# Performance work log

Hardware: AMD Instinct MI355X
Metric: run time of the kernel (lower is better)

## Reference

```python
import math
import jax, jax.numpy as jnp
import numpy as np

B = 128          # graphs per batch
N = 1024         # nodes per graph
E = 1048576      # total edges (avg degree 8)
F_IN = 64
NHID = 64
NCLS = 10
RATIO = 0.8


def setup_inputs() -> dict:
    key = jax.random.key(0)
    ks = jax.random.split(key, 24)
    x = jax.random.normal(ks[0], (B * N, F_IN), jnp.float32)
    # intra-graph random edges: graph id per edge, local src/dst
    epg = E // B
    gid = jnp.repeat(jnp.arange(B, dtype=jnp.int32), epg)
    src = gid * N + jax.random.randint(ks[1], (E,), 0, N, jnp.int32)
    dst = gid * N + jax.random.randint(ks[2], (E,), 0, N, jnp.int32)
    def lin(k, fi, fo):
        s = 1.0 / np.sqrt(fi)
        return jax.random.uniform(k, (fi, fo), jnp.float32, -s, s)
    p = {
        'W1': lin(ks[3], F_IN, NHID), 'b1': jnp.zeros((NHID,), jnp.float32),
        'Wp1': lin(ks[4], NHID, 1), 'bp1': jnp.zeros((1,), jnp.float32),
        'W2': lin(ks[5], NHID, NHID), 'b2': jnp.zeros((NHID,), jnp.float32),
        'Wp2': lin(ks[6], NHID, 1), 'bp2': jnp.zeros((1,), jnp.float32),
        'W3': lin(ks[7], NHID, NHID), 'b3': jnp.zeros((NHID,), jnp.float32),
        'Wp3': lin(ks[8], NHID, 1), 'bp3': jnp.zeros((1,), jnp.float32),
        'L1w': lin(ks[9], 2 * NHID, NHID), 'L1b': jnp.zeros((NHID,), jnp.float32),
        'L2w': lin(ks[10], NHID, NHID // 2), 'L2b': jnp.zeros((NHID // 2,), jnp.float32),
        'L3w': lin(ks[11], NHID // 2, NCLS), 'L3b': jnp.zeros((NCLS,), jnp.float32),
    }
    return dict(x=x, edge_src=src, edge_dst=dst, **p)


def gcn_conv(x, W, b, src, dst, emask, n):
    # PyG GCNConv: add self loops, symmetric deg normalization
    xw = x @ W
    ew = emask.astype(x.dtype)
    deg = jax.ops.segment_sum(ew, dst, num_segments=n) + 1.0  # +1 self loop
    dis = jax.lax.rsqrt(deg)
    norm = dis[src] * dis[dst] * ew
    agg = jax.ops.segment_sum(xw[src] * norm[:, None], dst, num_segments=n)
    agg = agg + xw * (dis * dis)[:, None]  # self-loop message
    return agg + b


def sag_pool(x, Wp, bp, src, dst, emask, n_cur):
    n_tot = B * n_cur
    k = int(math.ceil(RATIO * n_cur))
    score = gcn_conv(x, Wp, bp, src, dst, emask, n_tot)[:, 0]
    _, idx = jax.lax.top_k(score.reshape(B, n_cur), k)
    perm = (idx + (jnp.arange(B, dtype=jnp.int32) * n_cur)[:, None]).reshape(-1)
    xn = x[perm] * jnp.tanh(score[perm])[:, None]
    new_idx = jnp.full((n_tot,), -1, jnp.int32).at[perm].set(
        jnp.arange(B * k, dtype=jnp.int32))
    ns, nd = new_idx[src], new_idx[dst]
    valid = emask & (ns >= 0) & (nd >= 0)
    return xn, jnp.where(valid, ns, 0), jnp.where(valid, nd, 0), valid, k


def readout(x, k):
    xr = x.reshape(B, k, NHID)
    return jnp.concatenate([xr.max(axis=1), xr.mean(axis=1)], axis=1)


def reference(x, edge_src, edge_dst, W1, b1, Wp1, bp1, W2, b2, Wp2, bp2,
              W3, b3, Wp3, bp3, L1w, L1b, L2w, L2b, L3w, L3b):
    src = edge_src.astype(jnp.int32)
    dst = edge_dst.astype(jnp.int32)
    emask = jnp.ones((E,), bool)
    n = N
    h = jax.nn.relu(gcn_conv(x, W1, b1, src, dst, emask, B * n))
    h, src, dst, emask, n = sag_pool(h, Wp1, bp1, src, dst, emask, n)
    r1 = readout(h, n)
    h = jax.nn.relu(gcn_conv(h, W2, b2, src, dst, emask, B * n))
    h, src, dst, emask, n = sag_pool(h, Wp2, bp2, src, dst, emask, n)
    r2 = readout(h, n)
    h = jax.nn.relu(gcn_conv(h, W3, b3, src, dst, emask, B * n))
    h, src, dst, emask, n = sag_pool(h, Wp3, bp3, src, dst, emask, n)
    r3 = readout(h, n)
    z = r1 + r2 + r3
    z = jax.nn.relu(z @ L1w + L1b)          # dropout is identity in eval
    z = jax.nn.relu(z @ L2w + L2b)
    return jax.nn.log_softmax(z @ L3w + L3b, axis=-1)
```

## Files before the change

kernel.cpp:

```cpp
#include <hip/hip_runtime.h>
#include <math.h>

constexpr int B_  = 128;
constexpr int N_  = 1024;
constexpr int E_  = 1048576;
constexpr int BN_ = B_ * N_;
constexpr int EPG = E_ / B_;
constexpr int NSEG = 16;

typedef short v8s __attribute__((ext_vector_type(8)));
typedef float v4f __attribute__((ext_vector_type(4)));

__device__ __forceinline__ unsigned bf16_rne(unsigned u) {
    return (u + 0x7FFFu + ((u >> 16) & 1u)) >> 16;
}

__global__ __launch_bounds__(1024) void k_csr2(
        const int* __restrict__ src, const int* __restrict__ dst,
        const int* __restrict__ cum,
        int* __restrict__ srt, int* __restrict__ rowptr,
        float* __restrict__ dis, int n) {
    __shared__ int cnt[1024];
    __shared__ int cur[1024];
    __shared__ int cums[1024];
    __shared__ int wsum[17];
    int g = blockIdx.x, tid = threadIdx.x;
    int gb   = g * N_;
    int base = g * n;
    const int eb = g * EPG;

    cums[tid] = cum ? cum[gb + tid] : tid;
    cnt[tid] = 0;
    __syncthreads();
    for (int t = tid; t < EPG; t += 1024) {
        int s = cums[src[eb + t] - gb];
        int d = cums[dst[eb + t] - gb];
        if ((s | d) >= 0) atomicAdd(&cnt[d], 1);
    }
    __syncthreads();

    int c = (tid < n) ? cnt[tid] : 0;
    int v = c;
    int lane = tid & 63, wv = tid >> 6;
    #pragma unroll
    for (int off = 1; off < 64; off <<= 1) {
        int t = __shfl_up(v, off, 64);
        if (lane >= off) v += t;
    }
    if (lane == 63) wsum[wv] = v;
    __syncthreads();
    if (tid == 0) {
        int run = 0;
        #pragma unroll
        for (int i = 0; i < 16; ++i) { int t = wsum[i]; wsum[i] = run; run += t; }
        wsum[16] = run;
    }
    __syncthreads();
    int excl = v - c + wsum[wv];
    if (tid < n) {
        cur[tid] = excl;
        rowptr[g * (n + 1) + tid] = excl;
        dis[base + tid] = rsqrtf((float)c + 1.0f);
    }
    if (tid == 0) rowptr[g * (n + 1) + n] = wsum[16];
    __syncthreads();

    for (int t = tid; t < EPG; t += 1024) {
        int s = cums[src[eb + t] - gb];
        int d = cums[dst[eb + t] - gb];
        if ((s | d) < 0) continue;
        int pos = atomicAdd(&cur[d], 1);
        srt[eb + pos] = s;
    }
}

__global__ __launch_bounds__(1024) void k_wprep3(
        const float* __restrict__ W0, const float* __restrict__ W1,
        const float* __restrict__ W2, unsigned short* __restrict__ wfall) {
    const float* W = (blockIdx.x == 0) ? W0 : (blockIdx.x == 1) ? W1 : W2;
    unsigned short* wf = wfall + (size_t)blockIdx.x * 8192;
    int t = threadIdx.x;
    int l  = t & 63;
    int kk = (t >> 6) & 1;
    int c  = (t >> 7) & 3;
    int p  = (t >> 9) & 1;
    int col = c * 16 + (l & 15);
    int kbase = kk * 32 + (l >> 4) * 8;
    unsigned short o[8];
    #pragma unroll
    for (int j = 0; j < 8; ++j) {
        float w = W[(kbase + j) * 64 + col];
        unsigned u  = __float_as_uint(w);
        unsigned hi = bf16_rne(u);
        if (p == 0) o[j] = (unsigned short)hi;
        else {
            float lo = w - __uint_as_float(hi << 16);
            o[j] = (unsigned short)bf16_rne(__float_as_uint(lo));
        }
    }
    uint4 v;
    v.x = o[0] | ((unsigned)o[1] << 16);
    v.y = o[2] | ((unsigned)o[3] << 16);
    v.z = o[4] | ((unsigned)o[5] << 16);
    v.w = o[6] | ((unsigned)o[7] << 16);
    *reinterpret_cast<uint4*>(wf + (size_t)t * 8) = v;
}

__global__ __launch_bounds__(1024) void k_conv(
        const int* __restrict__ srt, const int* __restrict__ rowptr,
        const float* __restrict__ dis, const float* __restrict__ h,
        const int* __restrict__ perm, const float* __restrict__ ggate,
        const unsigned short* __restrict__ wf,
        const float* __restrict__ bias, const float* __restrict__ Wp,
        float* __restrict__ hout, float* __restrict__ saggq,
        int n, int rows) {
    extern __shared__ float lds[];
    float* xs   = lds;
    float* ps   = xs + n * 20;
    int*   lrp  = (int*)(ps + n);
    int*   lsrt = lrp + (n + 4);
    float* hs   = (float*)(lsrt + EPG);
    float* sdis = hs + 128 * 68;

    int g = blockIdx.x & 127, q = blockIdx.x >> 7;
    int foff = q * 16;
    int tid  = threadIdx.x;
    int base = g * n;

    for (int i = tid; i <= n; i += 1024) lrp[i] = rowptr[g * (n + 1) + i];
    __syncthreads();
    int total = lrp[n];
    const int* gsrt = srt + g * EPG;
    for (int i = tid; i < total; i += 1024) lsrt[i] = gsrt[i];

    int lane = tid & 63;
    v8s wh[2], wl[2];
    #pragma unroll
    for (int kk = 0; kk < 2; ++kk) {
        wh[kk] = *reinterpret_cast<const v8s*>(wf + (((size_t)((0*4 + q)*2 + kk))*64 + lane)*8);
        wl[kk] = *reinterpret_cast<const v8s*>(wf + (((size_t)((1*4 + q)*2 + kk))*64 + lane)*8);
    }

    int wave = tid >> 6;
    int m = lane & 15, b = lane >> 4;
    for (int c0 = 0; c0 < n; c0 += 128) {
        int ric = min(128, n - c0);
        __syncthreads();
        for (int i = tid; i < 128 * 16; i += 1024) {
            int row = i >> 4, s = i & 15;
            float4 v = {0.f, 0.f, 0.f, 0.f};
            if (row < ric) {
                if (perm) {
                    int pr   = perm[base + c0 + row];
                    float gt = ggate[base + c0 + row];
                    v = *reinterpret_cast<const float4*>(h + (size_t)pr * 64 + s * 4);
                    v.x *= gt; v.y *= gt; v.z *= gt; v.w *= gt;
                } else {
                    v = *reinterpret_cast<const float4*>(h + (size_t)(base + c0 + row) * 64 + s * 4);
                }
            }
            *reinterpret_cast<float4*>(&hs[row * 68 + s * 4]) = v;
        }
        if (tid < 128) sdis[tid] = (c0 + tid < n) ? dis[base + c0 + tid] : 0.f;
        __syncthreads();

        if (wave < 8 && wave * 16 < ric) {
            int lr0 = wave * 16;
            float f[16];
            *reinterpret_cast<float4*>(f)      = *reinterpret_cast<const float4*>(&hs[(lr0 + m) * 68 + b * 8]);
            *reinterpret_cast<float4*>(f + 4)  = *reinterpret_cast<const float4*>(&hs[(lr0 + m) * 68 + b * 8 + 4]);
            *reinterpret_cast<float4*>(f + 8)  = *reinterpret_cast<const float4*>(&hs[(lr0 + m) * 68 + 32 + b * 8]);
            *reinterpret_cast<float4*>(f + 12) = *reinterpret_cast<const float4*>(&hs[(lr0 + m) * 68 + 32 + b * 8 + 4]);
            v8s ah[2], al[2];
            #pragma unroll
            for (int ch = 0; ch < 2; ++ch) {
                #pragma unroll
                for (int j = 0; j < 8; ++j) {
                    float x = f[ch * 8 + j];
                    unsigned u  = __float_as_uint(x);
                    unsigned hi = bf16_rne(u);
                    float lo = x - __uint_as_float(hi << 16);
                    ah[ch][j] = (short)hi;
                    al[ch][j] = (short)bf16_rne(__float_as_uint(lo));
                }
            }
            v4f acc = {0.f, 0.f, 0.f, 0.f};
            acc = __builtin_amdgcn_mfma_f32_16x16x32_bf16(ah[0], wh[0], acc, 0, 0, 0);
            acc = __builtin_amdgcn_mfma_f32_16x16x32_bf16(ah[1], wh[1], acc, 0, 0, 0);
            acc = __builtin_amdgcn_mfma_f32_16x16x32_bf16(al[0], wh[0], acc, 0, 0, 0);
            acc = __builtin_amdgcn_mfma_f32_16x16x32_bf16(al[1], wh[1], acc, 0, 0, 0);
            acc = __builtin_amdgcn_mfma_f32_16x16x32_bf16(ah[0], wl[0], acc, 0, 0, 0);
            acc = __builtin_amdgcn_mfma_f32_16x16x32_bf16(ah[1], wl[1], acc, 0, 0, 0);
            acc = __builtin_amdgcn_mfma_f32_16x16x32_bf16(al[0], wl[0], acc, 0, 0, 0);
            acc = __builtin_amdgcn_mfma_f32_16x16x32_bf16(al[1], wl[1], acc, 0, 0, 0);
            #pragma unroll
            for (int reg = 0; reg < 4; ++reg) {
                int lr = lr0 + b * 4 + reg;
                if (c0 + lr < n) xs[(c0 + lr) * 20 + m] = acc[reg] * sdis[lr];
            }
        }
    }
    __syncthreads();

    int sub = tid & 3;
    float4 bq  = *reinterpret_cast<const float4*>(bias + foff + sub * 4);
    float4 wp4 = *reinterpret_cast<const float4*>(Wp   + foff + sub * 4);
    for (int row = tid >> 2; row < n; row += 256) {
        int s0 = lrp[row], s1 = lrp[row + 1];
        float4 acc = *reinterpret_cast<const float4*>(xs + row * 20 + sub * 4);
        for (int j = s0; j < s1; ++j) {
            int s = lsrt[j];
            const float4 v = *reinterpret_cast<const float4*>(xs + s * 20 + sub * 4);
            acc.x += v.x; acc.y += v.y; acc.z += v.z; acc.w += v.w;
        }
        float dsc = dis[base + row];
        float4 o;
        o.x = fmaxf(fmaf(dsc, acc.x, bq.x), 0.0f);
        o.y = fmaxf(fmaf(dsc, acc.y, bq.y), 0.0f);
        o.z = fmaxf(fmaf(dsc, acc.z, bq.z), 0.0f);
        o.w = fmaxf(fmaf(dsc, acc.w, bq.w), 0.0f);
        *reinterpret_cast<float4*>(hout + (size_t)(base + row) * 64 + foff + sub * 4) = o;
        float part = o.x * wp4.x + o.y * wp4.y + o.z * wp4.z + o.w * wp4.w;
        part += __shfl_xor(part, 1, 64);
        part += __shfl_xor(part, 2, 64);
        if (sub == 0) ps[row] = part * dsc;
    }
    __syncthreads();

    for (int row = tid; row < n; row += 1024) {
        float acc = ps[row];
        int s1 = lrp[row + 1];
        for (int j = lrp[row]; j < s1; ++j) acc += ps[lsrt[j]];
        saggq[(size_t)q * BN_ + base + row] = acc;
    }
}

__global__ __launch_bounds__(1024) void k_score_topk(
        const float* __restrict__ dis, const float* __restrict__ saggq,
        const float* __restrict__ bp, int n, int k,
        int* __restrict__ perm, float* __restrict__ ggate,
        int* __restrict__ cum, int do_compose) {
    __shared__ unsigned long long keys[1024];
    __shared__ int mark[1024];
    int g = blockIdx.x, tid = threadIdx.x;
    int base = g * n;
    float bp0 = bp[0];

    unsigned long long kv = 0ull;
    if (tid < n) {
        float s0 = saggq[0 * (size_t)BN_ + base + tid] + saggq[1 * (size_t)BN_ + base + tid]
                 + saggq[2 * (size_t)BN_ + base + tid] + saggq[3 * (size_t)BN_ + base + tid];
        float sag = dis[base + tid] * s0 + bp0;
        unsigned u  = __float_as_uint(sag);
        unsigned mk = (u & 0x80000000u) ? ~u : (u | 0x80000000u);
        kv = ((unsigned long long)mk << 32) | (unsigned)tid;
    }
    keys[tid] = kv;
    mark[tid] = -1;

    for (int size = 2; size <= 1024; size <<= 1) {
        for (int stride = size >> 1; stride > 0; stride >>= 1) {
            __syncthreads();
            if (tid < 512) {
                int a  = ((tid / stride) * (stride << 1)) + (tid & (stride - 1));
                int bx = a + stride;
                bool asc = ((a & size) == 0);
                unsigned long long ka = keys[a], kb = keys[bx];
                bool sw = asc ? (ka > kb) : (ka < kb);
                if (sw) { keys[a] = kb; keys[bx] = ka; }
            }
        }
    }
    __syncthreads();

    if (tid < k) {
        int j = tid;
        unsigned long long kvv = keys[1023 - j];
        int local   = (int)(kvv & 0xFFFFFFFFull);
        unsigned mk = (unsigned)(kvv >> 32);
        unsigned u  = (mk & 0x80000000u) ? (mk ^ 0x80000000u) : ~mk;
        int newg = g * k + j;
        perm[newg]  = base + local;
        ggate[newg] = tanhf(__uint_as_float(u));
        mark[local] = j;
    }
    __syncthreads();
    if (do_compose) {
        int gb = g * N_;
        int c = (do_compose == 1) ? tid : cum[gb + tid];
        cum[gb + tid] = (c >= 0) ? mark[c] : -1;
    }
}

__global__ __launch_bounds__(256) void k_readout_seg(
        const float* __restrict__ h, const int* __restrict__ perm,
        const float* __restrict__ ggate, int k, float* __restrict__ pz) {
    int g = blockIdx.x / NSEG, seg = blockIdx.x % NSEG;
    int ck = (k + NSEG - 1) / NSEG;
    int j0 = seg * ck;
    int j1 = min(k, j0 + ck);
    __shared__ float gate[64];
    __shared__ int   lperm[64];
    int tid = threadIdx.x;
    for (int j = j0 + tid; j < j1; j += 256) {
        lperm[j - j0] = perm[g * k + j];
        gate[j - j0]  = ggate[g * k + j];
    }
    __syncthreads();
    int lane = tid & 63, w = tid >> 6;
    float mx = -INFINITY, sm = 0.0f;
    for (int j = j0 + w; j < j1; j += 4) {
        float v = h[(size_t)lperm[j - j0] * 64 + lane] * gate[j - j0];
        mx = fmaxf(mx, v); sm += v;
    }
    __shared__ float smx[4][64], ssm[4][64];
    smx[w][lane] = mx; ssm[w][lane] = sm;
    __syncthreads();
    if (w == 0) {
        #pragma unroll
        for (int i = 1; i < 4; ++i) { mx = fmaxf(mx, smx[i][lane]); sm += ssm[i][lane]; }
        float* p = pz + ((size_t)g * NSEG + seg) * 128;
        p[lane]      = mx;
        p[64 + lane] = sm;
    }
}

__global__ __launch_bounds__(128) void k_mlp(const float* __restrict__ pz,
                      const float* __restrict__ L1w, const float* __restrict__ L1b,
                      const float* __restrict__ L2w, const float* __restrict__ L2b,
                      const float* __restrict__ L3w, const float* __restrict__ L3b,
                      float* __restrict__ out) {
    __shared__ float z[128], h1[64], h2[32], lg[10], lse;
    int g = blockIdx.x, tid = threadIdx.x;
    const float kinv[3] = {1.0f / 820.0f, 1.0f / 656.0f, 1.0f / 525.0f};
    float zv = 0.0f;
    if (tid < 64) {
        #pragma unroll
        for (int L = 0; L < 3; ++L) {
            const float* p = pz + (((size_t)L * B_ + g) * NSEG) * 128;
            float mx = -INFINITY;
            #pragma unroll
            for (int s = 0; s < NSEG; ++s) mx = fmaxf(mx, p[s * 128 + tid]);
            zv += mx;
        }
    } else {
        int f = tid - 64;
        #pragma unroll
        for (int L = 0; L < 3; ++L) {
            const float* p = pz + (((size_t)L * B_ + g) * NSEG) * 128;
            float sm = 0.0f;
            #pragma unroll
            for (int s = 0; s < NSEG; ++s) sm += p[s * 128 + 64 + f];
            zv += sm * kinv[L];
        }
    }
    z[tid] = zv;
    __syncthreads();
    if (tid < 64) {
        float acc = L1b[tid];
        for (int i = 0; i < 128; ++i) acc = fmaf(z[i], L1w[i * 64 + tid], acc);
        h1[tid] = fmaxf(acc, 0.0f);
    }
    __syncthreads();
    if (tid < 32) {
        float acc = L2b[tid];
        for (int i = 0; i < 64; ++i) acc = fmaf(h1[i], L2w[i * 32 + tid], acc);
        h2[tid] = fmaxf(acc, 0.0f);
    }
    __syncthreads();
    if (tid < 10) {
        float acc = L3b[tid];
        for (int i = 0; i < 32; ++i) acc = fmaf(h2[i], L3w[i * 10 + tid], acc);
        lg[tid] = acc;
    }
    __syncthreads();
    if (tid == 0) {
        float m = lg[0];
        for (int i = 1; i < 10; ++i) m = fmaxf(m, lg[i]);
        float s = 0.0f;
        for (int i = 0; i < 10; ++i) s += expf(lg[i] - m);
        lse = m + logf(s);
    }
    __syncthreads();
    if (tid < 10) out[g * 10 + tid] = lg[tid] - lse;
}

extern "C" void kernel_launch(void* const* d_in, const int* in_sizes, int n_in,
                              void* d_out, int out_size, void* d_ws, size_t ws_size,
                              hipStream_t stream) {
    const float* x    = (const float*)d_in[0];
    const int*   esrc = (const int*)d_in[1];
    const int*   edst = (const int*)d_in[2];
    const float* W [3] = {(const float*)d_in[3],  (const float*)d_in[7],  (const float*)d_in[11]};
    const float* bb[3] = {(const float*)d_in[4],  (const float*)d_in[8],  (const float*)d_in[12]};
    const float* Wp[3] = {(const float*)d_in[5],  (const float*)d_in[9],  (const float*)d_in[13]};
    const float* bp[3] = {(const float*)d_in[6],  (const float*)d_in[10], (const float*)d_in[14]};
    const float* L1w = (const float*)d_in[15];
    const float* L1b = (const float*)d_in[16];
    const float* L2w = (const float*)d_in[17];
    const float* L2b = (const float*)d_in[18];
    const float* L3w = (const float*)d_in[19];
    const float* L3b = (const float*)d_in[20];
    float* out = (float*)d_out;

    float* fws   = (float*)d_ws;
    float* agg   = fws;
    float* dis   = agg  + (size_t)BN_ * 64;
    float* saggq = dis  + BN_;
    float* ggate = saggq + 4 * (size_t)BN_;
    float* pz    = ggate + BN_;
    int*   perm   = (int*)(pz + 3 * B_ * NSEG * 128);
    int*   cum    = perm + BN_;
    int*   srt    = cum + BN_;
    int*   rowptr = srt + E_;
    unsigned short* wfrag = (unsigned short*)(rowptr + B_ * (N_ + 1));

    hipFuncSetAttribute(reinterpret_cast<const void*>(k_conv),
                        hipFuncAttributeMaxDynamicSharedMemorySize,
                        (22 * 1024 + 17028) * 4);

    k_wprep3<<<3, 1024, 0, stream>>>(W[0], W[1], W[2], wfrag);

    const int ks_[3] = {820, 656, 525};
    int n = N_;

    for (int L = 0; L < 3; ++L) {
        int rows = B_ * n;
        int k    = ks_[L];

        k_csr2<<<B_, 1024, 0, stream>>>(esrc, edst, (L == 0) ? nullptr : cum,
                                        srt, rowptr, dis, n);

        k_conv<<<B_ * 4, 1024, (size_t)(22 * n + 17028) * 4, stream>>>(
            srt, rowptr, dis,
            (L == 0) ? x : agg,
            (L == 0) ? nullptr : perm,
            (L == 0) ? nullptr : ggate,
            wfrag + (size_t)L * 8192, bb[L], Wp[L],
            agg, saggq, n, rows);

        k_score_topk<<<B_, 1024, 0, stream>>>(dis, saggq, bp[L], n, k,
                                              perm, ggate, cum, (L < 2) ? (L + 1) : 0);

        k_readout_seg<<<B_ * NSEG, 256, 0, stream>>>(agg, perm, ggate, k,
                                                     pz + (size_t)L * B_ * NSEG * 128);

        n = k;
    }

    k_mlp<<<B_, 128, 0, stream>>>(pz, L1w, L1b, L2w, L2b, L3w, L3b, out);
}
```

Before: 265.8 us.

## Shrink k_conv LDS footprint by streaming CSR from global and dropping staging tile

Rewrites k_conv to cut shared memory from about 22n+17028 floats to 20n. The edge list and row pointers are no longer copied into LDS; the gather loops read them directly from global memory. The staged h tile is removed, so each wave loads its 16-row tile straight from global into registers and reads dis from global. The partial-score array is packed into the spare 17th column of xs. This removes the chunked 128-row loop and its barriers and may allow more resident blocks per CU, at the cost of repeated uncoalesced global reads of the CSR indices inside the gather loops.

```diff
diff --git a/kernel.cpp b/kernel.cpp
--- a/kernel.cpp
+++ b/kernel.cpp
@@ -106,32 +106,21 @@
     *reinterpret_cast<uint4*>(wf + (size_t)t * 8) = v;
 }
 
-__global__ __launch_bounds__(1024) void k_conv(
+__global__ __launch_bounds__(1024, 8) void k_conv(
         const int* __restrict__ srt, const int* __restrict__ rowptr,
         const float* __restrict__ dis, const float* __restrict__ h,
         const int* __restrict__ perm, const float* __restrict__ ggate,
         const unsigned short* __restrict__ wf,
         const float* __restrict__ bias, const float* __restrict__ Wp,
-        float* __restrict__ hout, float* __restrict__ saggq,
-        int n, int rows) {
-    extern __shared__ float lds[];
-    float* xs   = lds;
-    float* ps   = xs + n * 20;
-    int*   lrp  = (int*)(ps + n);
-    int*   lsrt = lrp + (n + 4);
-    float* hs   = (float*)(lsrt + EPG);
-    float* sdis = hs + 128 * 68;
+        float* __restrict__ hout, float* __restrict__ saggq, int n) {
+    extern __shared__ float xs[];
 
     int g = blockIdx.x & 127, q = blockIdx.x >> 7;
     int foff = q * 16;
     int tid  = threadIdx.x;
     int base = g * n;
-
-    for (int i = tid; i <= n; i += 1024) lrp[i] = rowptr[g * (n + 1) + i];
-    __syncthreads();
-    int total = lrp[n];
+    const int* grp  = rowptr + g * (n + 1);
     const int* gsrt = srt + g * EPG;
-    for (int i = tid; i < total; i += 1024) lsrt[i] = gsrt[i];
 
     int lane = tid & 63;
     v8s wh[2], wl[2];
@@ -143,61 +132,55 @@
 
     int wave = tid >> 6;
     int m = lane & 15, b = lane >> 4;
-    for (int c0 = 0; c0 < n; c0 += 128) {
-        int ric = min(128, n - c0);
-        __syncthreads();
-        for (int i = tid; i < 128 * 16; i += 1024) {
-            int row = i >> 4, s = i & 15;
-            float4 v = {0.f, 0.f, 0.f, 0.f};
-            if (row < ric) {
-                if (perm) {
-                    int pr   = perm[base + c0 + row];
-                    float gt = ggate[base + c0 + row];
-                    v = *reinterpret_cast<const float4*>(h + (size_t)pr * 64 + s * 4);
-                    v.x *= gt; v.y *= gt; v.z *= gt; v.w *= gt;
-                } else {
-                    v = *reinterpret_cast<const float4*>(h + (size_t)(base + c0 + row) * 64 + s * 4);
-                }
+    int ntiles = (n + 15) >> 4;
+    for (int t = wave; t < ntiles; t += 16) {
+        int c0 = t * 16;
+        int arow = c0 + m;
+        float f[16];
+        if (arow < n) {
+            float gt = 1.0f;
+            size_t r;
+            if (perm) { r = (size_t)perm[base + arow]; gt = ggate[base + arow]; }
+            else       r = (size_t)(base + arow);
+            const float4* hrow = reinterpret_cast<const float4*>(h + r * 64);
+            float4 v0 = hrow[b * 2 + 0];
+            float4 v1 = hrow[b * 2 + 1];
+            float4 v2 = hrow[8 + b * 2 + 0];
+            float4 v3 = hrow[8 + b * 2 + 1];
+            f[0]=v0.x*gt; f[1]=v0.y*gt; f[2]=v0.z*gt; f[3]=v0.w*gt;
+            f[4]=v1.x*gt; f[5]=v1.y*gt; f[6]=v1.z*gt; f[7]=v1.w*gt;
+            f[8]=v2.x*gt; f[9]=v2.y*gt; f[10]=v2.z*gt; f[11]=v2.w*gt;
+            f[12]=v3.x*gt; f[13]=v3.y*gt; f[14]=v3.z*gt; f[15]=v3.w*gt;
+        } else {
+            #pragma unroll
+            for (int j = 0; j < 16; ++j) f[j] = 0.0f;
+        }
+        v8s ah[2], al[2];
+        #pragma unroll
+        for (int ch = 0; ch < 2; ++ch) {
+            #pragma unroll
+            for (int j = 0; j < 8; ++j) {
+                float x = f[ch * 8 + j];
+                unsigned u  = __float_as_uint(x);
+                unsigned hi = bf16_rne(u);
+                float lo = x - __uint_as_float(hi << 16);
+                ah[ch][j] = (short)hi;
+                al[ch][j] = (short)bf16_rne(__float_as_uint(lo));
             }
-            *reinterpret_cast<float4*>(&hs[row * 68 + s * 4]) = v;
-        }
-        if (tid < 128) sdis[tid] = (c0 + tid < n) ? dis[base + c0 + tid] : 0.f;
-        __syncthreads();
-
-        if (wave < 8 && wave * 16 < ric) {
-            int lr0 = wave * 16;
-            float f[16];
-            *reinterpret_cast<float4*>(f)      = *reinterpret_cast<const float4*>(&hs[(lr0 + m) * 68 + b * 8]);
-            *reinterpret_cast<float4*>(f + 4)  = *reinterpret_cast<const float4*>(&hs[(lr0 + m) * 68 + b * 8 + 4]);
-            *reinterpret_cast<float4*>(f + 8)  = *reinterpret_cast<const float4*>(&hs[(lr0 + m) * 68 + 32 + b * 8]);
-            *reinterpret_cast<float4*>(f + 12) = *reinterpret_cast<const float4*>(&hs[(lr0 + m) * 68 + 32 + b * 8 + 4]);
-            v8s ah[2], al[2];
-            #pragma unroll
-            for (int ch = 0; ch < 2; ++ch) {
-                #pragma unroll
-                for (int j = 0; j < 8; ++j) {
-                    float x = f[ch * 8 + j];
-                    unsigned u  = __float_as_uint(x);
-                    unsigned hi = bf16_rne(u);
-                    float lo = x - __uint_as_float(hi << 16);
-                    ah[ch][j] = (short)hi;
-                    al[ch][j] = (short)bf16_rne(__float_as_uint(lo));
-                }
-            }
-            v4f acc = {0.f, 0.f, 0.f, 0.f};
-            acc = __builtin_amdgcn_mfma_f32_16x16x32_bf16(ah[0], wh[0], acc, 0, 0, 0);
-            acc = __builtin_amdgcn_mfma_f32_16x16x32_bf16(ah[1], wh[1], acc, 0, 0, 0);
-            acc = __builtin_amdgcn_mfma_f32_16x16x32_bf16(al[0], wh[0], acc, 0, 0, 0);
-            acc = __builtin_amdgcn_mfma_f32_16x16x32_bf16(al[1], wh[1], acc, 0, 0, 0);
-            acc = __builtin_amdgcn_mfma_f32_16x16x32_bf16(ah[0], wl[0], acc, 0, 0, 0);
-            acc = __builtin_amdgcn_mfma_f32_16x16x32_bf16(ah[1], wl[1], acc, 0, 0, 0);
-            acc = __builtin_amdgcn_mfma_f32_16x16x32_bf16(al[0], wl[0], acc, 0, 0, 0);
-            acc = __builtin_amdgcn_mfma_f32_16x16x32_bf16(al[1], wl[1], acc, 0, 0, 0);
-            #pragma unroll
-            for (int reg = 0; reg < 4; ++reg) {
-                int lr = lr0 + b * 4 + reg;
-                if (c0 + lr < n) xs[(c0 + lr) * 20 + m] = acc[reg] * sdis[lr];
-            }
+        }
+        v4f acc = {0.f, 0.f, 0.f, 0.f};
+        acc = __builtin_amdgcn_mfma_f32_16x16x32_bf16(ah[0], wh[0], acc, 0, 0, 0);
+        acc = __builtin_amdgcn_mfma_f32_16x16x32_bf16(ah[1], wh[1], acc, 0, 0, 0);
+        acc = __builtin_amdgcn_mfma_f32_16x16x32_bf16(al[0], wh[0], acc, 0, 0, 0);
+        acc = __builtin_amdgcn_mfma_f32_16x16x32_bf16(al[1], wh[1], acc, 0, 0, 0);
+        acc = __builtin_amdgcn_mfma_f32_16x16x32_bf16(ah[0], wl[0], acc, 0, 0, 0);
+        acc = __builtin_amdgcn_mfma_f32_16x16x32_bf16(ah[1], wl[1], acc, 0, 0, 0);
+        acc = __builtin_amdgcn_mfma_f32_16x16x32_bf16(al[0], wl[0], acc, 0, 0, 0);
+        acc = __builtin_amdgcn_mfma_f32_16x16x32_bf16(al[1], wl[1], acc, 0, 0, 0);
+        #pragma unroll
+        for (int reg = 0; reg < 4; ++reg) {
+            int orow = c0 + b * 4 + reg;
+            if (orow < n) xs[orow * 20 + m] = acc[reg] * dis[base + orow];
         }
     }
     __syncthreads();
@@ -206,10 +189,10 @@
     float4 bq  = *reinterpret_cast<const float4*>(bias + foff + sub * 4);
     float4 wp4 = *reinterpret_cast<const float4*>(Wp   + foff + sub * 4);
     for (int row = tid >> 2; row < n; row += 256) {
-        int s0 = lrp[row], s1 = lrp[row + 1];
+        int s0 = grp[row], s1 = grp[row + 1];
         float4 acc = *reinterpret_cast<const float4*>(xs + row * 20 + sub * 4);
         for (int j = s0; j < s1; ++j) {
-            int s = lsrt[j];
+            int s = gsrt[j];
             const float4 v = *reinterpret_cast<const float4*>(xs + s * 20 + sub * 4);
             acc.x += v.x; acc.y += v.y; acc.z += v.z; acc.w += v.w;
         }
@@ -223,14 +206,14 @@
         float part = o.x * wp4.x + o.y * wp4.y + o.z * wp4.z + o.w * wp4.w;
         part += __shfl_xor(part, 1, 64);
         part += __shfl_xor(part, 2, 64);
-        if (sub == 0) ps[row] = part * dsc;
+        if (sub == 0) xs[row * 20 + 16] = part * dsc;
     }
     __syncthreads();
 
     for (int row = tid; row < n; row += 1024) {
-        float acc = ps[row];
-        int s1 = lrp[row + 1];
-        for (int j = lrp[row]; j < s1; ++j) acc += ps[lsrt[j]];
+        float acc = xs[row * 20 + 16];
+        int s1 = grp[row + 1];
+        for (int j = grp[row]; j < s1; ++j) acc += xs[gsrt[j] * 20 + 16];
         saggq[(size_t)q * BN_ + base + row] = acc;
     }
 }
@@ -416,8 +399,7 @@
     unsigned short* wfrag = (unsigned short*)(rowptr + B_ * (N_ + 1));
 
     hipFuncSetAttribute(reinterpret_cast<const void*>(k_conv),
-                        hipFuncAttributeMaxDynamicSharedMemorySize,
-                        (22 * 1024 + 17028) * 4);
+                        hipFuncAttributeMaxDynamicSharedMemorySize, 20 * 1024 * 4);
 
     k_wprep3<<<3, 1024, 0, stream>>>(W[0], W[1], W[2], wfrag);
 
@@ -425,19 +407,18 @@
     int n = N_;
 
     for (int L = 0; L < 3; ++L) {
-        int rows = B_ * n;
-        int k    = ks_[L];
+        int k = ks_[L];
 
         k_csr2<<<B_, 1024, 0, stream>>>(esrc, edst, (L == 0) ? nullptr : cum,
                                         srt, rowptr, dis, n);
 
-        k_conv<<<B_ * 4, 1024, (size_t)(22 * n + 17028) * 4, stream>>>(
+        k_conv<<<B_ * 4, 1024, (size_t)(20 * n) * 4, stream>>>(
             srt, rowptr, dis,
             (L == 0) ? x : agg,
             (L == 0) ? nullptr : perm,
             (L == 0) ? nullptr : ggate,
             wfrag + (size_t)L * 8192, bb[L], Wp[L],
-            agg, saggq, n, rows);
+            agg, saggq, n);
 
         k_score_topk<<<B_, 1024, 0, stream>>>(dis, saggq, bp[L], n, k,
                                               perm, ggate, cum, (L < 2) ? (L + 1) : 0);
```

Result: faster. 247.5 us (-6.9%).
